# Optimization experiments

Measured on AMD Instinct MI355X. Metric: run time of the kernel, lower is better.

Reference implementation:

```python
import jax, jax.numpy as jnp
import numpy as np


def setup_inputs() -> dict:
    key = jax.random.key(0)
    k1, k2 = jax.random.split(key)
    N, P, SMK, L = 256, 64, 2048, 32
    inp = jax.random.normal(k1, (N, P, SMK, 2), dtype=jnp.float32)
    # channel taps; in the original these are randn scaled by sqrt(power/2)
    cof = jax.random.normal(k2, (N, P, L, 2), dtype=jnp.float32) * 0.1
    return {"input": inp, "cof": cof, "M": 64}


def reference(input, cof, M):
    # input: (N, P, SMK, 2) real/imag stacked; cof: (N, P, L, 2)
    N, P, SMK, _ = input.shape
    L = cof.shape[2]
    sig = (input[..., 0] + 1j * input[..., 1]).reshape(N * P, SMK)   # complex64
    h = (cof[..., 0] + 1j * cof[..., 1]).reshape(N * P, L)
    # torch path: conv1d with time-reversed taps and padding=L-1 == FULL linear
    # convolution; four real convs == one complex conv.
    out_c = jax.vmap(lambda s, k: jnp.convolve(s, k, mode="full"))(sig, h)  # (N*P, SMK+L-1)
    output = jnp.stack([out_c.real, out_c.imag], axis=-1).reshape(N, P, SMK + L - 1, 2)
    # H_t = FFT of zero-padded taps along the tap axis (length M)
    cof_zp = jnp.pad(cof, ((0, 0), (0, 0), (0, M - L), (0, 0)))
    Hc = jnp.fft.fft(cof_zp[..., 0] + 1j * cof_zp[..., 1], axis=-1)  # (N, P, M)
    H_t = jnp.stack([Hc.real, Hc.imag], axis=-1)                      # (N, P, M, 2)
    return output, H_t
```

## Files before the change

### kernel.cpp

```cpp
#include <hip/hip_runtime.h>
#include <math.h>

#define SMK    2048
#define TAPS   32
#define OUTLEN (SMK + TAPS - 1)
#define PAD    32
#define SLOTS  (PAD + SMK + PAD)
#define MDFT   64

__device__ __forceinline__ int swz(int p) { return p ^ ((p >> 4) & 15); }

__global__ __launch_bounds__(256, 4)
void conv_kernel(const float* __restrict__ input,
                 const float* __restrict__ cof,
                 float* __restrict__ out0)
{
    __shared__ float2 s_sig[SLOTS];
    __shared__ float2 s_tap[TAPS];
    const int tid = threadIdx.x;
    const int row = blockIdx.x;

    const float4* gin = (const float4*)(input + (size_t)row * SMK * 2);
    #pragma unroll
    for (int k = 0; k < 4; ++k) {
        float4 v = gin[tid + 256 * k];
        int i0 = PAD + 2 * (tid + 256 * k);
        s_sig[swz(i0)]     = make_float2(v.x, v.y);
        s_sig[swz(i0 + 1)] = make_float2(v.z, v.w);
    }
    if (tid < PAD) {
        s_sig[swz(tid)] = make_float2(0.f, 0.f);
    } else if (tid < 2 * PAD) {
        s_sig[swz(PAD + SMK + (tid - PAD))] = make_float2(0.f, 0.f);
    }
    if (tid < TAPS) {
        const float2* ct = (const float2*)(cof + (size_t)row * TAPS * 2);
        s_tap[tid] = ct[tid];
    }
    __syncthreads();

    const int t0 = tid * 8;

    float2 win[39];
    #pragma unroll
    for (int m = 0; m < 39; ++m) win[m] = s_sig[swz(t0 + 1 + m)];

    float2 acc[8];
    #pragma unroll
    for (int k = 0; k < 8; ++k) acc[k] = make_float2(0.f, 0.f);

    #pragma unroll
    for (int l = 0; l < TAPS; ++l) {
        float2 h = s_tap[l];
        #pragma unroll
        for (int k = 0; k < 8; ++k) {
            float2 s = win[k + 31 - l];
            acc[k].x = fmaf(s.x, h.x, fmaf(-s.y, h.y, acc[k].x));
            acc[k].y = fmaf(s.x, h.y, fmaf( s.y, h.x, acc[k].y));
        }
    }

    float2* go = (float2*)(out0 + (size_t)row * OUTLEN * 2);
    #pragma unroll
    for (int k = 0; k < 8; ++k) go[t0 + k] = acc[k];

    if (tid < OUTLEN - SMK) {
        int t = SMK + tid;
        float2 a = make_float2(0.f, 0.f);
        #pragma unroll
        for (int l = 0; l < TAPS; ++l) {
            float2 h = s_tap[l];
            float2 s = s_sig[swz(t - l + PAD)];
            a.x = fmaf(s.x, h.x, fmaf(-s.y, h.y, a.x));
            a.y = fmaf(s.x, h.y, fmaf( s.y, h.x, a.y));
        }
        go[t] = a;
    }
}

__global__ __launch_bounds__(256)
void dft_kernel(const float* __restrict__ cof,
                float* __restrict__ out1)
{
    __shared__ float2 tw[MDFT];
    __shared__ float  taps[256];
    const int tid = threadIdx.x;
    const int r0  = blockIdx.x * 4;

    if (tid < MDFT) {
        float ang = -2.0f * (float)M_PI * (float)tid / (float)MDFT;
        tw[tid] = make_float2(cosf(ang), sinf(ang));
    }
    taps[tid] = cof[(size_t)r0 * TAPS * 2 + tid];
    __syncthreads();

    const int sub = tid >> 6;
    const int k   = tid & 63;
    const float2* h = (const float2*)&taps[sub * TAPS * 2];

    float2 a = make_float2(0.f, 0.f);
    #pragma unroll
    for (int l = 0; l < TAPS; ++l) {
        float2 hv = h[l];
        float2 w  = tw[(k * l) & (MDFT - 1)];
        a.x = fmaf(hv.x, w.x, fmaf(-hv.y, w.y, a.x));
        a.y = fmaf(hv.x, w.y, fmaf( hv.y, w.x, a.y));
    }
    ((float2*)out1)[(size_t)(r0 + sub) * MDFT + k] = a;
}

extern "C" void kernel_launch(void* const* d_in, const int* in_sizes, int n_in,
                              void* d_out, int out_size, void* d_ws, size_t ws_size,
                              hipStream_t stream)
{
    const float* input = (const float*)d_in[0];
    const float* cof   = (const float*)d_in[1];

    const int NP = in_sizes[0] / (SMK * 2);

    float* out0 = (float*)d_out;
    float* out1 = out0 + (size_t)NP * OUTLEN * 2;

    conv_kernel<<<NP, 256, 0, stream>>>(input, cof, out0);
    dft_kernel<<<NP / 4, 256, 0, stream>>>(cof, out1);
}
```

Baseline: 158.6 us.

## Fuse tap DFT into conv kernel and stage output through LDS for coalesced stores

Merges the separate DFT launch into the convolution kernel so the taps are read once and one launch is saved. Tap values are made wave-uniform via readfirstlane and held in scalar registers instead of being re-read from LDS each iteration. Conv results are staged in a swizzled LDS buffer and written out with thread-contiguous float2 stores, replacing each thread's strided 8-element writes. This adds about 16KB of LDS per block and an extra barrier, which may cut occupancy.

```diff
diff --git a/kernel.cpp b/kernel.cpp
--- a/kernel.cpp
+++ b/kernel.cpp
@@ -7,16 +7,26 @@
 #define PAD    32
 #define SLOTS  (PAD + SMK + PAD)
 #define MDFT   64
+#define NF4    1040
 
 __device__ __forceinline__ int swz(int p) { return p ^ ((p >> 4) & 15); }
+__device__ __forceinline__ int swz4(int s) { return s ^ ((s >> 3) & 7); }
+
+__device__ __forceinline__ float rfl(float x) {
+    return __int_as_float(__builtin_amdgcn_readfirstlane(__float_as_int(x)));
+}
 
 __global__ __launch_bounds__(256, 4)
 void conv_kernel(const float* __restrict__ input,
                  const float* __restrict__ cof,
-                 float* __restrict__ out0)
+                 float* __restrict__ out0,
+                 float* __restrict__ out1)
 {
     __shared__ float2 s_sig[SLOTS];
+    __shared__ float4 s_out[NF4];
     __shared__ float2 s_tap[TAPS];
+    __shared__ float2 s_tw[MDFT];
+
     const int tid = threadIdx.x;
     const int row = blockIdx.x;
 
@@ -31,13 +41,27 @@
     if (tid < PAD) {
         s_sig[swz(tid)] = make_float2(0.f, 0.f);
     } else if (tid < 2 * PAD) {
-        s_sig[swz(PAD + SMK + (tid - PAD))] = make_float2(0.f, 0.f);
+        s_sig[swz(SMK + tid)] = make_float2(0.f, 0.f);
     }
     if (tid < TAPS) {
         const float2* ct = (const float2*)(cof + (size_t)row * TAPS * 2);
         s_tap[tid] = ct[tid];
     }
+    if (tid >= 64 && tid < 128) {
+        int j = tid - 64;
+        float sv, cv;
+        __sincosf(-2.0f * (float)M_PI * (float)j / (float)MDFT, &sv, &cv);
+        s_tw[j] = make_float2(cv, sv);
+    }
     __syncthreads();
+
+    float hre[TAPS], him[TAPS];
+    #pragma unroll
+    for (int l = 0; l < TAPS; ++l) {
+        float2 h = s_tap[l];
+        hre[l] = rfl(h.x);
+        him[l] = rfl(h.y);
+    }
 
     const int t0 = tid * 8;
 
@@ -51,62 +75,62 @@
 
     #pragma unroll
     for (int l = 0; l < TAPS; ++l) {
-        float2 h = s_tap[l];
+        const float hr = hre[l];
+        const float hi = him[l];
         #pragma unroll
         for (int k = 0; k < 8; ++k) {
             float2 s = win[k + 31 - l];
-            acc[k].x = fmaf(s.x, h.x, fmaf(-s.y, h.y, acc[k].x));
-            acc[k].y = fmaf(s.x, h.y, fmaf( s.y, h.x, acc[k].y));
+            acc[k].x = fmaf(s.x, hr, fmaf(-s.y, hi, acc[k].x));
+            acc[k].y = fmaf(s.x, hi, fmaf( s.y, hr, acc[k].y));
         }
     }
 
-    float2* go = (float2*)(out0 + (size_t)row * OUTLEN * 2);
     #pragma unroll
-    for (int k = 0; k < 8; ++k) go[t0 + k] = acc[k];
+    for (int k = 0; k < 4; ++k) {
+        float4 v = make_float4(acc[2 * k].x, acc[2 * k].y,
+                               acc[2 * k + 1].x, acc[2 * k + 1].y);
+        s_out[swz4(4 * tid + k)] = v;
+    }
 
     if (tid < OUTLEN - SMK) {
-        int t = SMK + tid;
+        const int t = SMK + tid;
         float2 a = make_float2(0.f, 0.f);
         #pragma unroll
         for (int l = 0; l < TAPS; ++l) {
-            float2 h = s_tap[l];
             float2 s = s_sig[swz(t - l + PAD)];
-            a.x = fmaf(s.x, h.x, fmaf(-s.y, h.y, a.x));
-            a.y = fmaf(s.x, h.y, fmaf( s.y, h.x, a.y));
+            a.x = fmaf(s.x, hre[l], fmaf(-s.y, him[l], a.x));
+            a.y = fmaf(s.x, him[l], fmaf( s.y, hre[l], a.y));
         }
-        go[t] = a;
+        float2* so2 = (float2*)s_out;
+        so2[swz4(t >> 1) * 2 + (t & 1)] = a;
     }
-}
-
-__global__ __launch_bounds__(256)
-void dft_kernel(const float* __restrict__ cof,
-                float* __restrict__ out1)
-{
-    __shared__ float2 tw[MDFT];
-    __shared__ float  taps[256];
-    const int tid = threadIdx.x;
-    const int r0  = blockIdx.x * 4;
 
     if (tid < MDFT) {
-        float ang = -2.0f * (float)M_PI * (float)tid / (float)MDFT;
-        tw[tid] = make_float2(cosf(ang), sinf(ang));
+        const int k = tid;
+        float2 a = make_float2(0.f, 0.f);
+        #pragma unroll
+        for (int l = 0; l < TAPS; ++l) {
+            float2 w = s_tw[(k * l) & (MDFT - 1)];
+            a.x = fmaf(w.x, hre[l], fmaf(-w.y, him[l], a.x));
+            a.y = fmaf(w.y, hre[l], fmaf( w.x, him[l], a.y));
+        }
+        ((float2*)out1)[(size_t)row * MDFT + k] = a;
     }
-    taps[tid] = cof[(size_t)r0 * TAPS * 2 + tid];
+
     __syncthreads();
 
-    const int sub = tid >> 6;
-    const int k   = tid & 63;
-    const float2* h = (const float2*)&taps[sub * TAPS * 2];
-
-    float2 a = make_float2(0.f, 0.f);
+    const float2* so2 = (const float2*)s_out;
+    float2* go2 = (float2*)(out0 + (size_t)row * OUTLEN * 2);
     #pragma unroll
-    for (int l = 0; l < TAPS; ++l) {
-        float2 hv = h[l];
-        float2 w  = tw[(k * l) & (MDFT - 1)];
-        a.x = fmaf(hv.x, w.x, fmaf(-hv.y, w.y, a.x));
-        a.y = fmaf(hv.x, w.y, fmaf( hv.y, w.x, a.y));
+    for (int it = 0; it < 8; ++it) {
+        int s2 = tid + 256 * it;
+        go2[s2] = so2[swz4(s2 >> 1) * 2 + (s2 & 1)];
     }
-    ((float2*)out1)[(size_t)(r0 + sub) * MDFT + k] = a;
+    {
+        int s2 = tid + 2048;
+        if (s2 < OUTLEN)
+            go2[s2] = so2[swz4(s2 >> 1) * 2 + (s2 & 1)];
+    }
 }
 
 extern "C" void kernel_launch(void* const* d_in, const int* in_sizes, int n_in,
@@ -121,6 +145,5 @@
     float* out0 = (float*)d_out;
     float* out1 = out0 + (size_t)NP * OUTLEN * 2;
 
-    conv_kernel<<<NP, 256, 0, stream>>>(input, cof, out0);
-    dft_kernel<<<NP / 4, 256, 0, stream>>>(cof, out1);
+    conv_kernel<<<NP, 256, 0, stream>>>(input, cof, out0, out1);
 }
```

Measured after the change: 154.8 us. -2.4%, faster.
